# Kernel optimization log

Hardware: AMD Instinct MI355X
Metric: run time of the kernel (lower is better)

The kernel has to match this reference:

```python
import jax, jax.numpy as jnp
import numpy as np
import math

D_MODEL = 1024
N_HEADS = 16
N_AA = 25
SS_DIM = 8
B, L = 4, 1024


def setup_inputs() -> dict:
    key = jax.random.key(0)
    ks = jax.random.split(key, 16)
    xavier = lambda k, shape: jax.random.uniform(
        k, shape, jnp.float32, -1.0, 1.0) * math.sqrt(6.0 / (shape[0] + shape[1]))
    inp = {
        "x": jax.random.normal(ks[0], (B, L, D_MODEL), jnp.float32),
        "physics_features": jax.random.uniform(ks[1], (B, L * L), jnp.float32),
        "amino_acid_ids": jax.random.randint(ks[2], (B, L), 0, N_AA),
        "secondary_structure": jax.random.uniform(ks[3], (B, L, SS_DIM), jnp.float32),
        "Wq": xavier(ks[4], (D_MODEL, D_MODEL)),
        "Wk": xavier(ks[5], (D_MODEL, D_MODEL)),
        "Wv": xavier(ks[6], (D_MODEL, D_MODEL)),
        "Wo": xavier(ks[7], (D_MODEL, D_MODEL)),
        "bo": jnp.zeros((D_MODEL,), jnp.float32),
        "dist_bias": jax.random.normal(ks[8], (1, N_HEADS, 1, 1), jnp.float32) * 0.02,
        "inter_mat": jax.random.normal(ks[9], (N_AA, N_AA), jnp.float32) * 0.02,
        "ss_w": xavier(ks[10], (N_HEADS, SS_DIM)),
        "physics_scale": jnp.float32(1.0),
        "distance_decay": jnp.float32(2.0),
    }
    # torch init symmetrizes the interaction matrix once at construction
    inp["inter_mat"] = (inp["inter_mat"] + inp["inter_mat"].T) / 2
    return inp


def reference(x, physics_features, amino_acid_ids, secondary_structure,
              Wq, Wk, Wv, Wo, bo, dist_bias, inter_mat, ss_w,
              physics_scale, distance_decay):
    Bsz, Ls, D = x.shape
    H = N_HEADS
    dk = D // H

    def heads(t):  # [B,L,D] -> [B,H,L,dk]
        return t.reshape(Bsz, Ls, H, dk).transpose(0, 2, 1, 3)

    q = heads(x @ Wq.T)
    k = heads(x @ Wk.T)
    v = heads(x @ Wv.T)

    scores = jnp.einsum('bhid,bhjd->bhij', q, k) / math.sqrt(dk)

    # --- distance bias: -clamp(dist)^decay * sigmoid(scale), broadcast over heads
    dist = jnp.clip(physics_features[:, :Ls * Ls].reshape(Bsz, Ls, Ls), 0.1, 50.0)
    decay = jnp.clip(distance_decay, 0.1, 5.0)
    dist_pen = -(dist ** decay) * jax.nn.sigmoid(physics_scale)  # [B,L,L]

    # --- amino-acid interaction bias: symmetric matrix gather * 1/(1+|i-j|)
    sym = (inter_mat + inter_mat.T) / 2
    ids = jnp.clip(amino_acid_ids, 0, N_AA - 1)
    inter = sym[ids[:, :, None], ids[:, None, :]]  # [B,L,L]
    pos = jnp.arange(Ls, dtype=x.dtype)
    inter = inter * (1.0 / (1.0 + jnp.abs(pos[None, :] - pos[:, None])))

    # --- secondary-structure bias: sigmoid(<proj_i, proj_j>) - 0.5 (same for all heads)
    proj = secondary_structure @ ss_w.T  # [B,L,H]
    struct = jax.nn.sigmoid(jnp.einsum('bih,bjh->bij', proj, proj)) - 0.5

    physics_bias = (dist_pen + inter + struct)[:, None, :, :] + dist_bias  # [B,H,L,L]
    scores = scores + physics_bias

    probs = jax.nn.softmax(scores, axis=-1)
    ctx = jnp.einsum('bhij,bhjd->bhid', probs, v)
    ctx = ctx.transpose(0, 2, 1, 3).reshape(Bsz, Ls, D)
    return ctx @ Wo.T + bo
```

## Files before the change

### kernel.cpp

```cpp
#include <hip/hip_runtime.h>

#define L_SEQ 1024
#define DMODEL 1024

typedef __attribute__((ext_vector_type(8))) short short8;
typedef __attribute__((ext_vector_type(4))) short shortx4;
typedef __attribute__((ext_vector_type(4))) float floatx4;

__device__ inline float bf2f(short s) {
    union { unsigned int u; float f; } v;
    v.u = ((unsigned int)(unsigned short)s) << 16;
    return v.f;
}
__device__ inline short f2bf(float f) {
    union { float f; unsigned int u; } v; v.f = f;
    unsigned int r = v.u + 0x7fff + ((v.u >> 16) & 1);
    return (short)(r >> 16);
}
__device__ inline void gload_lds16(const short* g, short* l) {
    __builtin_amdgcn_global_load_lds(
        (const __attribute__((address_space(1))) void*)g,
        (__attribute__((address_space(3))) void*)l, 16, 0, 0);
}

__global__ __launch_bounds__(256) void cvt_kernel(const float* __restrict__ src,
                                                  short* __restrict__ dst) {
    int idx = blockIdx.x * 256 + threadIdx.x;
    const float4* p = (const float4*)src + idx * 2;
    float4 a = p[0], b = p[1];
    short8 r;
    r[0] = f2bf(a.x); r[1] = f2bf(a.y); r[2] = f2bf(a.z); r[3] = f2bf(a.w);
    r[4] = f2bf(b.x); r[5] = f2bf(b.y); r[6] = f2bf(b.z); r[7] = f2bf(b.w);
    *(short8*)(dst + idx * 8) = r;
}

__global__ __launch_bounds__(256) void proj_kernel(const float* __restrict__ ss,
                                                   const float* __restrict__ ssw,
                                                   float* __restrict__ proj) {
    int idx = blockIdx.x * 256 + threadIdx.x;
    int h = idx & 15;
    int bl = idx >> 4;
    float s = 0.f;
#pragma unroll
    for (int d = 0; d < 8; ++d)
        s += ss[bl * 8 + d] * ssw[h * 8 + d];
    proj[bl * 16 + h] = s;
}

__global__ __launch_bounds__(256) void bias_kernel(const float* __restrict__ pf,
                                                   const int* __restrict__ ids,
                                                   const float* __restrict__ im,
                                                   const float* __restrict__ proj,
                                                   const float* __restrict__ ps,
                                                   const float* __restrict__ dd,
                                                   short* __restrict__ biasT) {
    int ti = blockIdx.x;
    int jc = blockIdx.y;
    int b  = blockIdx.z;
    int t = threadIdx.x;
    int iq = t >> 6, lane = t & 63;
    float decay = fminf(fmaxf(dd[0], 0.1f), 5.0f);
    float psig = 1.f / (1.f + __expf(-ps[0]));

    __shared__ float pi[16][16];
    __shared__ float interrow[16][25];
    {
        int row = t >> 4, col = t & 15;
        pi[row][col] = proj[(((b << 10) + ti * 16 + row) << 4) + col];
        for (int e = t; e < 16 * 25; e += 256) {
            int il = e / 25, c = e - il * 25;
            int id_i = min(max(ids[(b << 10) + ti * 16 + il], 0), 24);
            interrow[il][c] = 0.5f * (im[id_i * 25 + c] + im[c * 25 + id_i]);
        }
    }
    __syncthreads();

    int j0 = jc * 256 + lane * 4;
    float4 pfv[4];
#pragma unroll
    for (int ir = 0; ir < 4; ++ir) {
        int i = ti * 16 + iq * 4 + ir;
        pfv[ir] = *(const float4*)(pf + (b << 20) + (i << 10) + j0);
    }
    int4 idj4 = *(const int4*)(ids + (b << 10) + j0);
    int idj[4] = {min(max(idj4.x, 0), 24), min(max(idj4.y, 0), 24),
                  min(max(idj4.z, 0), 24), min(max(idj4.w, 0), 24)};

    int tj = j0 >> 4, jf0 = j0 & 15;
    short* outp = biasT + ((((b << 6) + ti) << 6) + tj) * 256 + (iq * 16 + jf0) * 4;
#pragma unroll
    for (int e = 0; e < 4; ++e) {
        int j = j0 + e;
        const float4* pj4 = (const float4*)(proj + (((b << 10) + j) << 4));
        float4 p0 = pj4[0], p1 = pj4[1], p2 = pj4[2], p3 = pj4[3];
        float pfe = (e == 0) ? 0.f : 0.f;
        shortx4 o;
#pragma unroll
        for (int ir = 0; ir < 4; ++ir) {
            int i = ti * 16 + iq * 4 + ir;
            float dvr = (e == 0) ? pfv[ir].x : (e == 1) ? pfv[ir].y : (e == 2) ? pfv[ir].z : pfv[ir].w;
            float dist = fminf(fmaxf(dvr, 0.1f), 50.0f);
            float dp = -__expf(decay * __logf(dist)) * psig;
            int il = iq * 4 + ir;
            float inter = interrow[il][idj[e]] / (1.0f + fabsf((float)(i - j)));
            const float* pir = pi[il];
            float dot = pir[0] * p0.x + pir[1] * p0.y + pir[2] * p0.z + pir[3] * p0.w
                      + pir[4] * p1.x + pir[5] * p1.y + pir[6] * p1.z + pir[7] * p1.w
                      + pir[8] * p2.x + pir[9] * p2.y + pir[10] * p2.z + pir[11] * p2.w
                      + pir[12] * p3.x + pir[13] * p3.y + pir[14] * p3.z + pir[15] * p3.w;
            float st = 1.f / (1.f + __expf(-dot)) - 0.5f;
            o[ir] = f2bf(dp + inter + st);
        }
        *(shortx4*)(outp + e * 4) = o;
        (void)pfe;
    }
}

__global__ __launch_bounds__(256) void gemm_qkv(const short* __restrict__ xb,
                                                const short* __restrict__ Wb,
                                                short* __restrict__ Q,
                                                short* __restrict__ K,
                                                short* __restrict__ Vt) {
    __shared__ __align__(16) short As[128 * 32];
    __shared__ __align__(16) short Bs[128 * 32];
    int t = threadIdx.x;
    int wave = t >> 6, lane = t & 63, fr = lane & 15, quad = lane >> 4;
    int wm = (wave & 1) * 64, wn = (wave >> 1) * 64;
    int m0 = blockIdx.x * 128, n0 = blockIdx.y * 128;
    const short* Ag = xb + (m0 + (t >> 2)) * DMODEL + (t & 3) * 8;
    const short* Bg = Wb + (n0 + (t >> 2)) * DMODEL + (t & 3) * 8;
    short* Asd = As + t * 8;
    short* Bsd = Bs + t * 8;
    floatx4 acc[4][4] = {};
    for (int k0 = 0; k0 < DMODEL; k0 += 32) {
        __syncthreads();
        gload_lds16(Ag + k0, Asd);
        gload_lds16(Ag + 64 * DMODEL + k0, Asd + 2048);
        gload_lds16(Bg + k0, Bsd);
        gload_lds16(Bg + 64 * DMODEL + k0, Bsd + 2048);
        __syncthreads();
        short8 a[4], b[4];
#pragma unroll
        for (int i = 0; i < 4; ++i) {
            a[i] = *(const short8*)(As + (wm + i * 16 + fr) * 32 + quad * 8);
            b[i] = *(const short8*)(Bs + (wn + i * 16 + fr) * 32 + quad * 8);
        }
#pragma unroll
        for (int i = 0; i < 4; ++i)
#pragma unroll
            for (int j = 0; j < 4; ++j)
                acc[i][j] = __builtin_amdgcn_mfma_f32_16x16x32_bf16(a[i], b[j], acc[i][j], 0, 0, 0);
    }
#pragma unroll
    for (int i = 0; i < 4; ++i)
#pragma unroll
        for (int j = 0; j < 4; ++j)
#pragma unroll
            for (int r = 0; r < 4; ++r) {
                int m = m0 + wm + i * 16 + quad * 4 + r;
                int n = n0 + wn + j * 16 + fr;
                int b_ = m >> 10, ii = m & 1023;
                int mode = n >> 10, nn = n & 1023;
                int h = nn >> 6, d = nn & 63;
                float v = acc[i][j][r];
                if (mode == 0)
                    Q[((b_ * 16 + h) * L_SEQ + ii) * 64 + d] = f2bf(v * 0.125f);
                else if (mode == 1)
                    K[((b_ * 16 + h) * L_SEQ + ii) * 64 + d] = f2bf(v);
                else
                    Vt[((b_ * 16 + h) * 64 + d) * L_SEQ + ii] = f2bf(v);
            }
}

__global__ __launch_bounds__(256) void gemm_out(const short* __restrict__ ctx,
                                                const short* __restrict__ Wob,
                                                const float* __restrict__ bo,
                                                float* __restrict__ out) {
    __shared__ __align__(16) short As[128 * 32];
    __shared__ __align__(16) short Bs[128 * 32];
    int t = threadIdx.x;
    int wave = t >> 6, lane = t & 63, fr = lane & 15, quad = lane >> 4;
    int wm = (wave & 1) * 64, wn = (wave >> 1) * 64;
    int m0 = blockIdx.x * 128, n0 = blockIdx.y * 128;
    const short* Ag = ctx + (m0 + (t >> 2)) * DMODEL + (t & 3) * 8;
    const short* Bg = Wob + (n0 + (t >> 2)) * DMODEL + (t & 3) * 8;
    short* Asd = As + t * 8;
    short* Bsd = Bs + t * 8;
    floatx4 acc[4][4] = {};
    for (int k0 = 0; k0 < DMODEL; k0 += 32) {
        __syncthreads();
        gload_lds16(Ag + k0, Asd);
        gload_lds16(Ag + 64 * DMODEL + k0, Asd + 2048);
        gload_lds16(Bg + k0, Bsd);
        gload_lds16(Bg + 64 * DMODEL + k0, Bsd + 2048);
        __syncthreads();
        short8 a[4], b[4];
#pragma unroll
        for (int i = 0; i < 4; ++i) {
            a[i] = *(const short8*)(As + (wm + i * 16 + fr) * 32 + quad * 8);
            b[i] = *(const short8*)(Bs + (wn + i * 16 + fr) * 32 + quad * 8);
        }
#pragma unroll
        for (int i = 0; i < 4; ++i)
#pragma unroll
            for (int j = 0; j < 4; ++j)
                acc[i][j] = __builtin_amdgcn_mfma_f32_16x16x32_bf16(a[i], b[j], acc[i][j], 0, 0, 0);
    }
#pragma unroll
    for (int i = 0; i < 4; ++i)
#pragma unroll
        for (int j = 0; j < 4; ++j)
#pragma unroll
            for (int r = 0; r < 4; ++r) {
                int m = m0 + wm + i * 16 + quad * 4 + r;
                int n = n0 + wn + j * 16 + fr;
                out[m * DMODEL + n] = acc[i][j][r] + bo[n];
            }
}

#define KSTR 72
#define VSTR 136
#define PSTR 136
__global__ __launch_bounds__(256, 2) void attn_kernel(const short* __restrict__ Q,
                                                      const short* __restrict__ K,
                                                      const short* __restrict__ Vt,
                                                      const short* __restrict__ biasT,
                                                      short* __restrict__ ctx) {
    __shared__ __align__(16) short Ks[128 * KSTR];
    __shared__ __align__(16) short Vs[64 * VSTR];
    __shared__ __align__(16) short Ps[4 * 2 * 16 * PSTR];
    int bh = blockIdx.x;
    int b = bh >> 4, h = bh & 15;
    int i0 = blockIdx.y * 128;
    int t = threadIdx.x;
    int w = t >> 6, lane = t & 63, fr = lane & 15, quad = lane >> 4;
    const short* Kg = K + (bh << 16);
    const short* Vg = Vt + (bh << 16);
    short* myP = Ps + w * (2 * 16 * PSTR);
    int tib[2];
    tib[0] = (((b << 6) + (i0 >> 4) + w * 2) << 6);
    tib[1] = tib[0] + 64;

    short8 qf[2][2];
#pragma unroll
    for (int it = 0; it < 2; ++it) {
        const short8* qp = (const short8*)(Q + ((bh << 10) + i0 + w * 32 + it * 16 + fr) * 64 + quad * 8);
        qf[it][0] = qp[0];
        qf[it][1] = qp[4];
    }
    float psum[2][4] = {};
    floatx4 pv[2][4] = {};

    short8 kreg[4], vreg[4];
#pragma unroll
    for (int s = 0; s < 4; ++s) {
        int seg = s * 256 + t;
        kreg[s] = *(const short8*)(Kg + ((seg >> 3)) * 64 + (seg & 7) * 8);
        vreg[s] = *(const short8*)(Vg + (seg >> 4) * 1024 + (seg & 15) * 8);
    }

    for (int jc = 0; jc < 8; ++jc) {
        if (jc) __syncthreads();
#pragma unroll
        for (int s = 0; s < 4; ++s) {
            int seg = s * 256 + t;
            *(short8*)(Ks + (seg >> 3) * KSTR + (seg & 7) * 8) = kreg[s];
            *(short8*)(Vs + (seg >> 4) * VSTR + (seg & 15) * 8) = vreg[s];
        }
        __syncthreads();
        if (jc < 7) {
#pragma unroll
            for (int s = 0; s < 4; ++s) {
                int seg = s * 256 + t;
                kreg[s] = *(const short8*)(Kg + ((jc + 1) * 128 + (seg >> 3)) * 64 + (seg & 7) * 8);
                vreg[s] = *(const short8*)(Vg + (seg >> 4) * 1024 + (jc + 1) * 128 + (seg & 15) * 8);
            }
        }
        shortx4 bfv[2][8];
#pragma unroll
        for (int it = 0; it < 2; ++it)
#pragma unroll
            for (int jt = 0; jt < 8; ++jt)
                bfv[it][jt] = *(const shortx4*)(biasT + ((tib[it] + jc * 8 + jt) << 8) + lane * 4);
        floatx4 sc[2][8];
#pragma unroll
        for (int jt = 0; jt < 8; ++jt) {
            short8 kb0 = *(const short8*)(Ks + (jt * 16 + fr) * KSTR + quad * 8);
            short8 kb1 = *(const short8*)(Ks + (jt * 16 + fr) * KSTR + 32 + quad * 8);
#pragma unroll
            for (int it = 0; it < 2; ++it) {
                floatx4 a = {0.f, 0.f, 0.f, 0.f};
                a = __builtin_amdgcn_mfma_f32_16x16x32_bf16(qf[it][0], kb0, a, 0, 0, 0);
                a = __builtin_amdgcn_mfma_f32_16x16x32_bf16(qf[it][1], kb1, a, 0, 0, 0);
                sc[it][jt] = a;
            }
        }
#pragma unroll
        for (int it = 0; it < 2; ++it)
#pragma unroll
            for (int jt = 0; jt < 8; ++jt)
#pragma unroll
                for (int r = 0; r < 4; ++r) {
                    float e = __expf(sc[it][jt][r] + bf2f(bfv[it][jt][r]));
                    psum[it][r] += e;
                    myP[(it * 16 + quad * 4 + r) * PSTR + jt * 16 + fr] = f2bf(e);
                }
#pragma unroll
        for (int ks = 0; ks < 4; ++ks) {
            short8 pa[2], vb[4];
#pragma unroll
            for (int it = 0; it < 2; ++it)
                pa[it] = *(const short8*)(myP + (it * 16 + fr) * PSTR + ks * 32 + quad * 8);
#pragma unroll
            for (int dt = 0; dt < 4; ++dt)
                vb[dt] = *(const short8*)(Vs + (dt * 16 + fr) * VSTR + ks * 32 + quad * 8);
#pragma unroll
            for (int it = 0; it < 2; ++it)
#pragma unroll
                for (int dt = 0; dt < 4; ++dt)
                    pv[it][dt] = __builtin_amdgcn_mfma_f32_16x16x32_bf16(pa[it], vb[dt], pv[it][dt], 0, 0, 0);
        }
    }
#pragma unroll
    for (int it = 0; it < 2; ++it)
#pragma unroll
        for (int r = 0; r < 4; ++r) {
#pragma unroll
            for (int mask = 8; mask >= 1; mask >>= 1)
                psum[it][r] += __shfl_xor(psum[it][r], mask);
        }
#pragma unroll
    for (int it = 0; it < 2; ++it)
#pragma unroll
        for (int dt = 0; dt < 4; ++dt)
#pragma unroll
            for (int r = 0; r < 4; ++r) {
                int i = i0 + w * 32 + it * 16 + quad * 4 + r;
                ctx[((b << 10) + i) * DMODEL + h * 64 + dt * 16 + fr] = f2bf(pv[it][dt][r] / psum[it][r]);
            }
}

extern "C" void kernel_launch(void* const* d_in, const int* in_sizes, int n_in,
                              void* d_out, int out_size, void* d_ws, size_t ws_size,
                              hipStream_t stream) {
    const float* x   = (const float*)d_in[0];
    const float* pf  = (const float*)d_in[1];
    const int*   ids = (const int*)d_in[2];
    const float* ss  = (const float*)d_in[3];
    const float* Wq  = (const float*)d_in[4];
    const float* Wk  = (const float*)d_in[5];
    const float* Wv  = (const float*)d_in[6];
    const float* Wo  = (const float*)d_in[7];
    const float* bo  = (const float*)d_in[8];
    const float* im  = (const float*)d_in[10];
    const float* ssw = (const float*)d_in[11];
    const float* ps  = (const float*)d_in[12];
    const float* dd  = (const float*)d_in[13];
    float* out = (float*)d_out;

    char* ws = (char*)d_ws;
    short* xb    = (short*)(ws);
    short* biasT = (short*)(ws);
    short* Wob   = (short*)(ws);
    short* Q     = (short*)(ws + (8u  << 20));
    short* K     = (short*)(ws + (16u << 20));
    short* Vt    = (short*)(ws + (24u << 20));
    short* Wb    = (short*)(ws + (32u << 20));
    short* ctx   = (short*)(ws + (32u << 20));
    float* proj  = (float*)(ws + (38u << 20));

    hipLaunchKernelGGL(cvt_kernel, dim3(2048), dim3(256), 0, stream, x, xb);
    hipLaunchKernelGGL(cvt_kernel, dim3(512), dim3(256), 0, stream, Wq, Wb);
    hipLaunchKernelGGL(cvt_kernel, dim3(512), dim3(256), 0, stream, Wk, Wb + (1u << 20));
    hipLaunchKernelGGL(cvt_kernel, dim3(512), dim3(256), 0, stream, Wv, Wb + (2u << 20));
    hipLaunchKernelGGL(proj_kernel, dim3(256), dim3(256), 0, stream, ss, ssw, proj);
    hipLaunchKernelGGL(gemm_qkv, dim3(32, 24), dim3(256), 0, stream, xb, Wb, Q, K, Vt);
    hipLaunchKernelGGL(bias_kernel, dim3(64, 4, 4), dim3(256), 0, stream,
                       pf, ids, im, proj, ps, dd, biasT);
    hipLaunchKernelGGL(attn_kernel, dim3(64, 8), dim3(256), 0, stream,
                       Q, K, Vt, biasT, ctx);
    hipLaunchKernelGGL(cvt_kernel, dim3(512), dim3(256), 0, stream, Wo, Wob);
    hipLaunchKernelGGL(gemm_out, dim3(32, 8), dim3(256), 0, stream, ctx, Wob, bo, out);
}
```

Before: 236.5 us.

## Fuse conversion launches, use exp2 with folded log2e, halve attention query tile

Merges the four bf16 conversion launches and the structure projection into a single kernel to cut launch overhead. Folds log2(e) into the Q scale and the bias so softmax can use exp2 directly. Shrinks the attention tile from 128 to 64 query rows per block (one 16-row tile per wave), doubling the grid and raising the occupancy target to 3 blocks. The smaller tile means K/V tiles are loaded and reused across fewer query rows, so global traffic for K/V rises.

```diff
diff --git a/kernel.cpp b/kernel.cpp
--- a/kernel.cpp
+++ b/kernel.cpp
@@ -2,6 +2,7 @@
 
 #define L_SEQ 1024
 #define DMODEL 1024
+#define LOG2E 1.4426950408889634f
 
 typedef __attribute__((ext_vector_type(8))) short short8;
 typedef __attribute__((ext_vector_type(4))) short shortx4;
@@ -23,28 +24,39 @@
         (__attribute__((address_space(3))) void*)l, 16, 0, 0);
 }
 
-__global__ __launch_bounds__(256) void cvt_kernel(const float* __restrict__ src,
-                                                  short* __restrict__ dst) {
-    int idx = blockIdx.x * 256 + threadIdx.x;
-    const float4* p = (const float4*)src + idx * 2;
-    float4 a = p[0], b = p[1];
-    short8 r;
-    r[0] = f2bf(a.x); r[1] = f2bf(a.y); r[2] = f2bf(a.z); r[3] = f2bf(a.w);
-    r[4] = f2bf(b.x); r[5] = f2bf(b.y); r[6] = f2bf(b.z); r[7] = f2bf(b.w);
-    *(short8*)(dst + idx * 8) = r;
-}
-
-__global__ __launch_bounds__(256) void proj_kernel(const float* __restrict__ ss,
-                                                   const float* __restrict__ ssw,
-                                                   float* __restrict__ proj) {
-    int idx = blockIdx.x * 256 + threadIdx.x;
-    int h = idx & 15;
-    int bl = idx >> 4;
-    float s = 0.f;
-#pragma unroll
-    for (int d = 0; d < 8; ++d)
-        s += ss[bl * 8 + d] * ssw[h * 8 + d];
-    proj[bl * 16 + h] = s;
+__global__ __launch_bounds__(256) void cvt_all(const float* __restrict__ x,
+                                               const float* __restrict__ Wq,
+                                               const float* __restrict__ Wk,
+                                               const float* __restrict__ Wv,
+                                               const float* __restrict__ ss,
+                                               const float* __restrict__ ssw,
+                                               short* __restrict__ xb,
+                                               short* __restrict__ Wb,
+                                               float* __restrict__ proj) {
+    int bid = blockIdx.x;
+    if (bid < 3584) {
+        const float* src; short* dst; int off;
+        if (bid < 2048)      { src = x;  dst = xb;               off = bid; }
+        else if (bid < 2560) { src = Wq; dst = Wb;               off = bid - 2048; }
+        else if (bid < 3072) { src = Wk; dst = Wb + (1u << 20);  off = bid - 2560; }
+        else                 { src = Wv; dst = Wb + (2u << 20);  off = bid - 3072; }
+        int idx = off * 256 + threadIdx.x;
+        const float4* p = (const float4*)src + idx * 2;
+        float4 a = p[0], b = p[1];
+        short8 r;
+        r[0] = f2bf(a.x); r[1] = f2bf(a.y); r[2] = f2bf(a.z); r[3] = f2bf(a.w);
+        r[4] = f2bf(b.x); r[5] = f2bf(b.y); r[6] = f2bf(b.z); r[7] = f2bf(b.w);
+        *(short8*)(dst + idx * 8) = r;
+    } else {
+        int idx = (bid - 3584) * 256 + threadIdx.x;
+        int h = idx & 15;
+        int bl = idx >> 4;
+        float s = 0.f;
+#pragma unroll
+        for (int d = 0; d < 8; ++d)
+            s += ss[bl * 8 + d] * ssw[h * 8 + d];
+        proj[bl * 16 + h] = s;
+    }
 }
 
 __global__ __launch_bounds__(256) void bias_kernel(const float* __restrict__ pf,
@@ -93,7 +105,6 @@
         int j = j0 + e;
         const float4* pj4 = (const float4*)(proj + (((b << 10) + j) << 4));
         float4 p0 = pj4[0], p1 = pj4[1], p2 = pj4[2], p3 = pj4[3];
-        float pfe = (e == 0) ? 0.f : 0.f;
         shortx4 o;
 #pragma unroll
         for (int ir = 0; ir < 4; ++ir) {
@@ -109,10 +120,9 @@
                       + pir[8] * p2.x + pir[9] * p2.y + pir[10] * p2.z + pir[11] * p2.w
                       + pir[12] * p3.x + pir[13] * p3.y + pir[14] * p3.z + pir[15] * p3.w;
             float st = 1.f / (1.f + __expf(-dot)) - 0.5f;
-            o[ir] = f2bf(dp + inter + st);
+            o[ir] = f2bf((dp + inter + st) * LOG2E);
         }
         *(shortx4*)(outp + e * 4) = o;
-        (void)pfe;
     }
 }
 
@@ -164,12 +174,23 @@
                 int h = nn >> 6, d = nn & 63;
                 float v = acc[i][j][r];
                 if (mode == 0)
-                    Q[((b_ * 16 + h) * L_SEQ + ii) * 64 + d] = f2bf(v * 0.125f);
+                    Q[((b_ * 16 + h) * L_SEQ + ii) * 64 + d] = f2bf(v * (0.125f * LOG2E));
                 else if (mode == 1)
                     K[((b_ * 16 + h) * L_SEQ + ii) * 64 + d] = f2bf(v);
                 else
                     Vt[((b_ * 16 + h) * 64 + d) * L_SEQ + ii] = f2bf(v);
             }
+}
+
+__global__ __launch_bounds__(256) void cvt_kernel(const float* __restrict__ src,
+                                                  short* __restrict__ dst) {
+    int idx = blockIdx.x * 256 + threadIdx.x;
+    const float4* p = (const float4*)src + idx * 2;
+    float4 a = p[0], b = p[1];
+    short8 r;
+    r[0] = f2bf(a.x); r[1] = f2bf(a.y); r[2] = f2bf(a.z); r[3] = f2bf(a.w);
+    r[4] = f2bf(b.x); r[5] = f2bf(b.y); r[6] = f2bf(b.z); r[7] = f2bf(b.w);
+    *(short8*)(dst + idx * 8) = r;
 }
 
 __global__ __launch_bounds__(256) void gemm_out(const short* __restrict__ ctx,
@@ -221,41 +242,35 @@
 #define KSTR 72
 #define VSTR 136
 #define PSTR 136
-__global__ __launch_bounds__(256, 2) void attn_kernel(const short* __restrict__ Q,
+__global__ __launch_bounds__(256, 3) void attn_kernel(const short* __restrict__ Q,
                                                       const short* __restrict__ K,
                                                       const short* __restrict__ Vt,
                                                       const short* __restrict__ biasT,
                                                       short* __restrict__ ctx) {
     __shared__ __align__(16) short Ks[128 * KSTR];
     __shared__ __align__(16) short Vs[64 * VSTR];
-    __shared__ __align__(16) short Ps[4 * 2 * 16 * PSTR];
+    __shared__ __align__(16) short Ps[4 * 16 * PSTR];
     int bh = blockIdx.x;
     int b = bh >> 4, h = bh & 15;
-    int i0 = blockIdx.y * 128;
+    int i0 = blockIdx.y * 64;
     int t = threadIdx.x;
     int w = t >> 6, lane = t & 63, fr = lane & 15, quad = lane >> 4;
     const short* Kg = K + (bh << 16);
     const short* Vg = Vt + (bh << 16);
-    short* myP = Ps + w * (2 * 16 * PSTR);
-    int tib[2];
-    tib[0] = (((b << 6) + (i0 >> 4) + w * 2) << 6);
-    tib[1] = tib[0] + 64;
-
-    short8 qf[2][2];
-#pragma unroll
-    for (int it = 0; it < 2; ++it) {
-        const short8* qp = (const short8*)(Q + ((bh << 10) + i0 + w * 32 + it * 16 + fr) * 64 + quad * 8);
-        qf[it][0] = qp[0];
-        qf[it][1] = qp[4];
-    }
-    float psum[2][4] = {};
-    floatx4 pv[2][4] = {};
+    short* myP = Ps + w * (16 * PSTR);
+    int tib = (((b << 6) + (i0 >> 4) + w) << 6);
+
+    const short8* qp = (const short8*)(Q + ((bh << 10) + i0 + w * 16 + fr) * 64 + quad * 8);
+    short8 qf0 = qp[0], qf1 = qp[4];
+
+    float psum[4] = {};
+    floatx4 pv[4] = {};
 
     short8 kreg[4], vreg[4];
 #pragma unroll
     for (int s = 0; s < 4; ++s) {
         int seg = s * 256 + t;
-        kreg[s] = *(const short8*)(Kg + ((seg >> 3)) * 64 + (seg & 7) * 8);
+        kreg[s] = *(const short8*)(Kg + (seg >> 3) * 64 + (seg & 7) * 8);
         vreg[s] = *(const short8*)(Vg + (seg >> 4) * 1024 + (seg & 15) * 8);
     }
 
@@ -276,68 +291,51 @@
                 vreg[s] = *(const short8*)(Vg + (seg >> 4) * 1024 + (jc + 1) * 128 + (seg & 15) * 8);
             }
         }
-        shortx4 bfv[2][8];
-#pragma unroll
-        for (int it = 0; it < 2; ++it)
-#pragma unroll
-            for (int jt = 0; jt < 8; ++jt)
-                bfv[it][jt] = *(const shortx4*)(biasT + ((tib[it] + jc * 8 + jt) << 8) + lane * 4);
-        floatx4 sc[2][8];
+        shortx4 bfv[8];
+#pragma unroll
+        for (int jt = 0; jt < 8; ++jt)
+            bfv[jt] = *(const shortx4*)(biasT + ((tib + jc * 8 + jt) << 8) + lane * 4);
+        floatx4 sc[8];
 #pragma unroll
         for (int jt = 0; jt < 8; ++jt) {
             short8 kb0 = *(const short8*)(Ks + (jt * 16 + fr) * KSTR + quad * 8);
             short8 kb1 = *(const short8*)(Ks + (jt * 16 + fr) * KSTR + 32 + quad * 8);
-#pragma unroll
-            for (int it = 0; it < 2; ++it) {
-                floatx4 a = {0.f, 0.f, 0.f, 0.f};
-                a = __builtin_amdgcn_mfma_f32_16x16x32_bf16(qf[it][0], kb0, a, 0, 0, 0);
-                a = __builtin_amdgcn_mfma_f32_16x16x32_bf16(qf[it][1], kb1, a, 0, 0, 0);
-                sc[it][jt] = a;
-            }
-        }
-#pragma unroll
-        for (int it = 0; it < 2; ++it)
-#pragma unroll
-            for (int jt = 0; jt < 8; ++jt)
-#pragma unroll
-                for (int r = 0; r < 4; ++r) {
-                    float e = __expf(sc[it][jt][r] + bf2f(bfv[it][jt][r]));
-                    psum[it][r] += e;
-                    myP[(it * 16 + quad * 4 + r) * PSTR + jt * 16 + fr] = f2bf(e);
-                }
+            floatx4 a = {0.f, 0.f, 0.f, 0.f};
+            a = __builtin_amdgcn_mfma_f32_16x16x32_bf16(qf0, kb0, a, 0, 0, 0);
+            a = __builtin_amdgcn_mfma_f32_16x16x32_bf16(qf1, kb1, a, 0, 0, 0);
+            sc[jt] = a;
+        }
+#pragma unroll
+        for (int jt = 0; jt < 8; ++jt)
+#pragma unroll
+            for (int r = 0; r < 4; ++r) {
+                float e = exp2f(sc[jt][r] + bf2f(bfv[jt][r]));
+                psum[r] += e;
+                myP[(quad * 4 + r) * PSTR + jt * 16 + fr] = f2bf(e);
+            }
 #pragma unroll
         for (int ks = 0; ks < 4; ++ks) {
-            short8 pa[2], vb[4];
-#pragma unroll
-            for (int it = 0; it < 2; ++it)
-                pa[it] = *(const short8*)(myP + (it * 16 + fr) * PSTR + ks * 32 + quad * 8);
-#pragma unroll
-            for (int dt = 0; dt < 4; ++dt)
-                vb[dt] = *(const short8*)(Vs + (dt * 16 + fr) * VSTR + ks * 32 + quad * 8);
-#pragma unroll
-            for (int it = 0; it < 2; ++it)
-#pragma unroll
-                for (int dt = 0; dt < 4; ++dt)
-                    pv[it][dt] = __builtin_amdgcn_mfma_f32_16x16x32_bf16(pa[it], vb[dt], pv[it][dt], 0, 0, 0);
-        }
-    }
-#pragma unroll
-    for (int it = 0; it < 2; ++it)
+            short8 pa = *(const short8*)(myP + fr * PSTR + ks * 32 + quad * 8);
+#pragma unroll
+            for (int dt = 0; dt < 4; ++dt) {
+                short8 vb = *(const short8*)(Vs + (dt * 16 + fr) * VSTR + ks * 32 + quad * 8);
+                pv[dt] = __builtin_amdgcn_mfma_f32_16x16x32_bf16(pa, vb, pv[dt], 0, 0, 0);
+            }
+        }
+    }
+#pragma unroll
+    for (int r = 0; r < 4; ++r) {
+#pragma unroll
+        for (int mask = 8; mask >= 1; mask >>= 1)
+            psum[r] += __shfl_xor(psum[r], mask);
+    }
+#pragma unroll
+    for (int dt = 0; dt < 4; ++dt)
 #pragma unroll
         for (int r = 0; r < 4; ++r) {
-#pragma unroll
-            for (int mask = 8; mask >= 1; mask >>= 1)
-                psum[it][r] += __shfl_xor(psum[it][r], mask);
-        }
-#pragma unroll
-    for (int it = 0; it < 2; ++it)
-#pragma unroll
-        for (int dt = 0; dt < 4; ++dt)
-#pragma unroll
-            for (int r = 0; r < 4; ++r) {
-                int i = i0 + w * 32 + it * 16 + quad * 4 + r;
-                ctx[((b << 10) + i) * DMODEL + h * 64 + dt * 16 + fr] = f2bf(pv[it][dt][r] / psum[it][r]);
-            }
+            int i = i0 + w * 16 + quad * 4 + r;
+            ctx[((b << 10) + i) * DMODEL + h * 64 + dt * 16 + fr] = f2bf(pv[dt][r] / psum[r]);
+        }
 }
 
 extern "C" void kernel_launch(void* const* d_in, const int* in_sizes, int n_in,
@@ -369,15 +367,12 @@
     short* ctx   = (short*)(ws + (32u << 20));
     float* proj  = (float*)(ws + (38u << 20));
 
-    hipLaunchKernelGGL(cvt_kernel, dim3(2048), dim3(256), 0, stream, x, xb);
-    hipLaunchKernelGGL(cvt_kernel, dim3(512), dim3(256), 0, stream, Wq, Wb);
-    hipLaunchKernelGGL(cvt_kernel, dim3(512), dim3(256), 0, stream, Wk, Wb + (1u << 20));
-    hipLaunchKernelGGL(cvt_kernel, dim3(512), dim3(256), 0, stream, Wv, Wb + (2u << 20));
-    hipLaunchKernelGGL(proj_kernel, dim3(256), dim3(256), 0, stream, ss, ssw, proj);
+    hipLaunchKernelGGL(cvt_all, dim3(3840), dim3(256), 0, stream,
+                       x, Wq, Wk, Wv, ss, ssw, xb, Wb, proj);
     hipLaunchKernelGGL(gemm_qkv, dim3(32, 24), dim3(256), 0, stream, xb, Wb, Q, K, Vt);
     hipLaunchKernelGGL(bias_kernel, dim3(64, 4, 4), dim3(256), 0, stream,
                        pf, ids, im, proj, ps, dd, biasT);
-    hipLaunchKernelGGL(attn_kernel, dim3(64, 8), dim3(256), 0, stream,
+    hipLaunchKernelGGL(attn_kernel, dim3(64, 16), dim3(256), 0, stream,
                        Q, K, Vt, biasT, ctx);
     hipLaunchKernelGGL(cvt_kernel, dim3(512), dim3(256), 0, stream, Wo, Wob);
     hipLaunchKernelGGL(gemm_out, dim3(32, 8), dim3(256), 0, stream, ctx, Wob, bo, out);
```

Measured after the change: 238.0 us. About the same (+0.6%).
